# Performance work log

Hardware: AMD Instinct MI355X
Metric: run time of the kernel (lower is better)

The kernel has to match this reference:

```python
import jax, jax.numpy as jnp
import numpy as np

N_NODES = 50000
HEADS = 8
NEG_SLOPE = 0.2


def _gat_conv(x, W, a_src, a_dst, b, src, dst, n_nodes):
    """PyG GATConv forward, concat=False (mean over heads), self-loops already in (src, dst)."""
    H, C = a_src.shape
    xl = (x @ W).reshape(n_nodes, H, C)                      # [N, H, C]
    alpha_src = jnp.einsum('nhc,hc->nh', xl, a_src)          # [N, H]
    alpha_dst = jnp.einsum('nhc,hc->nh', xl, a_dst)          # [N, H]
    alpha = jax.nn.leaky_relu(alpha_src[src] + alpha_dst[dst], NEG_SLOPE)  # [E, H]
    # segment softmax over edges grouped by destination node
    amax = jax.ops.segment_max(alpha, dst, num_segments=n_nodes)           # [N, H]
    amax = jnp.where(jnp.isfinite(amax), amax, jnp.zeros_like(amax))
    ex = jnp.exp(alpha - jax.lax.stop_gradient(amax)[dst])                  # [E, H]
    denom = jax.ops.segment_sum(ex, dst, num_segments=n_nodes)             # [N, H]
    coef = ex / (denom[dst] + 1e-16)                                        # [E, H]
    msg = xl[src] * coef[:, :, None]                                        # [E, H, C]
    out = jax.ops.segment_sum(msg, dst, num_segments=n_nodes)              # [N, H, C]
    return out.mean(axis=1) + b                                             # [N, C]


def setup_inputs() -> dict:
    key = jax.random.key(0)
    ks = jax.random.split(key, 12)
    in_feats, h_feats, out_feats = 256, 64, 64
    n_edges = 800000
    x = jax.random.normal(ks[0], (N_NODES, in_feats), dtype=jnp.float32)
    edge_index = jax.random.randint(ks[1], (2, n_edges), 0, N_NODES, dtype=jnp.int64)
    # Glorot-ish init for weights
    def glorot(k, shape, fan):
        return jax.random.normal(k, shape, dtype=jnp.float32) * (1.0 / np.sqrt(fan))
    W1 = glorot(ks[2], (in_feats, HEADS * h_feats), in_feats)
    a_src1 = glorot(ks[3], (HEADS, h_feats), h_feats)
    a_dst1 = glorot(ks[4], (HEADS, h_feats), h_feats)
    b1 = jnp.zeros((h_feats,), dtype=jnp.float32)
    W2 = glorot(ks[5], (h_feats, HEADS * out_feats), h_feats)
    a_src2 = glorot(ks[6], (HEADS, out_feats), out_feats)
    a_dst2 = glorot(ks[7], (HEADS, out_feats), out_feats)
    b2 = jnp.zeros((out_feats,), dtype=jnp.float32)
    return {"x": x, "edge_index": edge_index,
            "W1": W1, "a_src1": a_src1, "a_dst1": a_dst1, "b1": b1,
            "W2": W2, "a_src2": a_src2, "a_dst2": a_dst2, "b2": b2}


def reference(x, edge_index, W1, a_src1, a_dst1, b1, W2, a_src2, a_dst2, b2):
    n = x.shape[0]
    # PyG GATConv add_self_loops=True (default): append self loops
    loops = jnp.arange(n, dtype=edge_index.dtype)
    src = jnp.concatenate([edge_index[0], loops])
    dst = jnp.concatenate([edge_index[1], loops])
    # F.dropout(p=0.6) is identity in eval mode
    h = _gat_conv(x, W1, a_src1, a_dst1, b1, src, dst, n)
    h = jax.nn.relu(h)
    out = _gat_conv(h, W2, a_src2, a_dst2, b2, src, dst, n)
    return out
```

## Files before the change

kernel.cpp:

```cpp
#include <hip/hip_runtime.h>

#define NN 50000
#define MPAD 50048
#define HD 8
#define CD 64
#define NHF 512
#define SCAN_B 256
#define NBLK ((NN + SCAN_B - 1) / SCAN_B)

typedef __attribute__((ext_vector_type(8))) short short8v;
typedef __attribute__((ext_vector_type(8))) unsigned short us8;
typedef __attribute__((ext_vector_type(4))) unsigned short us4;
typedef __attribute__((ext_vector_type(4))) float f32x4;
typedef __attribute__((ext_vector_type(8))) _Float16 h8;

__device__ inline unsigned short f32_to_bf16(float f) {
    unsigned int u = __float_as_uint(f);
    unsigned int r = (u + 0x7fffu + ((u >> 16) & 1u)) >> 16;
    return (unsigned short)r;
}
__device__ inline float bf16_to_f32(unsigned short h) {
    return __uint_as_float(((unsigned int)h) << 16);
}

__global__ void k_init_cnt(int* __restrict__ cnt) {
    int i = blockIdx.x * 256 + threadIdx.x;
    if (i < NN) cnt[i] = 1;
}

__global__ void k_hist(const int* __restrict__ dst, int E, int* __restrict__ cnt) {
    int e = blockIdx.x * 256 + threadIdx.x;
    if (e < E) atomicAdd(&cnt[dst[e]], 1);
}

__global__ __launch_bounds__(SCAN_B) void k_block_sums(const int* __restrict__ cnt,
                                                       int* __restrict__ bsums) {
    __shared__ int sdata[4];
    int i = blockIdx.x * SCAN_B + threadIdx.x;
    int v = (i < NN) ? cnt[i] : 0;
#pragma unroll
    for (int off = 1; off < 64; off <<= 1) v += __shfl_xor(v, off);
    if ((threadIdx.x & 63) == 0) sdata[threadIdx.x >> 6] = v;
    __syncthreads();
    if (threadIdx.x == 0) bsums[blockIdx.x] = sdata[0] + sdata[1] + sdata[2] + sdata[3];
}

__global__ __launch_bounds__(SCAN_B) void k_scan_bsums(const int* __restrict__ bsums,
                                                       int* __restrict__ boffs, int nblk) {
    __shared__ int tmp[SCAN_B];
    int tid = threadIdx.x;
    int v = (tid < nblk) ? bsums[tid] : 0;
    tmp[tid] = v;
    __syncthreads();
    for (int off = 1; off < SCAN_B; off <<= 1) {
        int t = (tid >= off) ? tmp[tid - off] : 0;
        __syncthreads();
        tmp[tid] += t;
        __syncthreads();
    }
    if (tid < nblk) boffs[tid] = tmp[tid] - v;
}

__global__ __launch_bounds__(SCAN_B) void k_emit(const int* __restrict__ cnt,
                                                 const int* __restrict__ boffs,
                                                 int* __restrict__ row_ptr,
                                                 int* __restrict__ cursor,
                                                 int* __restrict__ csr_src) {
    __shared__ int tmp[SCAN_B];
    int tid = threadIdx.x;
    int i = blockIdx.x * SCAN_B + tid;
    int v = (i < NN) ? cnt[i] : 0;
    tmp[tid] = v;
    __syncthreads();
    for (int off = 1; off < SCAN_B; off <<= 1) {
        int t = (tid >= off) ? tmp[tid - off] : 0;
        __syncthreads();
        tmp[tid] += t;
        __syncthreads();
    }
    int base = boffs[blockIdx.x] + tmp[tid] - v;
    if (i < NN) {
        row_ptr[i] = base;
        csr_src[base] = i;
        cursor[i] = base + 1;
        if (i == NN - 1) row_ptr[NN] = base + v;
    }
}

__global__ void k_scatter(const int* __restrict__ src, const int* __restrict__ dst,
                          int E, int* __restrict__ cursor, int* __restrict__ csr_src) {
    int e = blockIdx.x * 256 + threadIdx.x;
    if (e < E) {
        int pos = atomicAdd(&cursor[dst[e]], 1);
        csr_src[pos] = src[e];
    }
}

__global__ void k_split_bt(const float* __restrict__ B, unsigned short* __restrict__ bht,
                           unsigned short* __restrict__ blt, int K) {
    int idx = blockIdx.x * 256 + threadIdx.x;
    if (idx < K * NHF) {
        int k = idx >> 9, n = idx & 511;
        float v = B[idx];
        unsigned short hb = f32_to_bf16(v);
        float l = v - bf16_to_f32(hb);
        blt[n * K + k] = f32_to_bf16(l);
        bht[n * K + k] = hb;
    }
}

#define BM 128
#define BN 256
#define BKF 32
#define LDK 40

template<int SPLIT>
__global__ __launch_bounds__(512) void k_gemm(
    const float* __restrict__ Af,
    const unsigned short* __restrict__ Aht,
    const unsigned short* __restrict__ Alt,
    const unsigned short* __restrict__ Bht,
    const unsigned short* __restrict__ Blt,
    const float* __restrict__ a_src, const float* __restrict__ a_dst,
    _Float16* __restrict__ C, float* __restrict__ asrc_out, float* __restrict__ adst_out,
    int M, int K)
{
    __shared__ unsigned short Ash[BM][LDK];
    __shared__ unsigned short Asl[BM][LDK];
    __shared__ unsigned short Bsh[BN][LDK];
    __shared__ unsigned short Bsl[BN][LDK];

    const int t = threadIdx.x;
    const int lane = t & 63;
    const int wid = t >> 6;
    const int wr = wid >> 2;
    const int wc = wid & 3;
    const int bm = blockIdx.x * BM;
    const int bn = blockIdx.y * BN;
    const int l15 = lane & 15;
    const int lg = lane >> 4;

    f32x4 acc[4][4];
#pragma unroll
    for (int mi = 0; mi < 4; ++mi)
#pragma unroll
        for (int ni = 0; ni < 4; ++ni)
            acc[mi][ni] = (f32x4){0.f, 0.f, 0.f, 0.f};

    const int srowA = t >> 2;
    const int skcA  = (t & 3) * 8;
    const int srowB = t >> 1;
    const int skcB  = (t & 1) * 16;

    for (int k0 = 0; k0 < K; k0 += BKF) {
        __syncthreads();
        if (SPLIT) {
            const int gr = bm + srowA;
            if (gr < M) {
                const float* ga = Af + (size_t)gr * K + k0 + skcA;
                float4 v0 = *(const float4*)ga;
                float4 v1 = *(const float4*)(ga + 4);
                us4 h0, l0, h1, l1;
                h0.x = f32_to_bf16(v0.x); l0.x = f32_to_bf16(v0.x - bf16_to_f32(h0.x));
                h0.y = f32_to_bf16(v0.y); l0.y = f32_to_bf16(v0.y - bf16_to_f32(h0.y));
                h0.z = f32_to_bf16(v0.z); l0.z = f32_to_bf16(v0.z - bf16_to_f32(h0.z));
                h0.w = f32_to_bf16(v0.w); l0.w = f32_to_bf16(v0.w - bf16_to_f32(h0.w));
                h1.x = f32_to_bf16(v1.x); l1.x = f32_to_bf16(v1.x - bf16_to_f32(h1.x));
                h1.y = f32_to_bf16(v1.y); l1.y = f32_to_bf16(v1.y - bf16_to_f32(h1.y));
                h1.z = f32_to_bf16(v1.z); l1.z = f32_to_bf16(v1.z - bf16_to_f32(h1.z));
                h1.w = f32_to_bf16(v1.w); l1.w = f32_to_bf16(v1.w - bf16_to_f32(h1.w));
                *(us4*)&Ash[srowA][skcA]     = h0;
                *(us4*)&Ash[srowA][skcA + 4] = h1;
                *(us4*)&Asl[srowA][skcA]     = l0;
                *(us4*)&Asl[srowA][skcA + 4] = l1;
            } else {
                us4 z = (us4){0, 0, 0, 0};
                *(us4*)&Ash[srowA][skcA]     = z;
                *(us4*)&Ash[srowA][skcA + 4] = z;
                *(us4*)&Asl[srowA][skcA]     = z;
                *(us4*)&Asl[srowA][skcA + 4] = z;
            }
        } else {
            const unsigned short* gah = Aht + (size_t)(bm + srowA) * K + k0 + skcA;
            const unsigned short* gal = Alt + (size_t)(bm + srowA) * K + k0 + skcA;
            *(us8*)&Ash[srowA][skcA] = *(const us8*)gah;
            *(us8*)&Asl[srowA][skcA] = *(const us8*)gal;
        }
        {
            const unsigned short* gbh = Bht + (size_t)(bn + srowB) * K + k0 + skcB;
            const unsigned short* gbl = Blt + (size_t)(bn + srowB) * K + k0 + skcB;
            *(us8*)&Bsh[srowB][skcB]     = *(const us8*)gbh;
            *(us8*)&Bsh[srowB][skcB + 8] = *(const us8*)(gbh + 8);
            *(us8*)&Bsl[srowB][skcB]     = *(const us8*)gbl;
            *(us8*)&Bsl[srowB][skcB + 8] = *(const us8*)(gbl + 8);
        }
        __syncthreads();

        short8v ah[4], al[4], bh[4], bl[4];
#pragma unroll
        for (int i = 0; i < 4; ++i) {
            ah[i] = *(const short8v*)&Ash[wr * 64 + i * 16 + l15][lg * 8];
            al[i] = *(const short8v*)&Asl[wr * 64 + i * 16 + l15][lg * 8];
            bh[i] = *(const short8v*)&Bsh[wc * 64 + i * 16 + l15][lg * 8];
            bl[i] = *(const short8v*)&Bsl[wc * 64 + i * 16 + l15][lg * 8];
        }
#pragma unroll
        for (int mi = 0; mi < 4; ++mi)
#pragma unroll
            for (int ni = 0; ni < 4; ++ni) {
                acc[mi][ni] = __builtin_amdgcn_mfma_f32_16x16x32_bf16(ah[mi], bh[ni], acc[mi][ni], 0, 0, 0);
                acc[mi][ni] = __builtin_amdgcn_mfma_f32_16x16x32_bf16(ah[mi], bl[ni], acc[mi][ni], 0, 0, 0);
                acc[mi][ni] = __builtin_amdgcn_mfma_f32_16x16x32_bf16(al[mi], bh[ni], acc[mi][ni], 0, 0, 0);
            }
    }

    const int head_w = (bn >> 6) + wc;
    float ca[4], cd[4];
#pragma unroll
    for (int ni = 0; ni < 4; ++ni) {
        ca[ni] = a_src[head_w * 64 + ni * 16 + l15];
        cd[ni] = a_dst[head_w * 64 + ni * 16 + l15];
    }
#pragma unroll
    for (int mi = 0; mi < 4; ++mi) {
#pragma unroll
        for (int r = 0; r < 4; ++r) {
            int row = bm + wr * 64 + mi * 16 + lg * 4 + r;
            float ps = 0.f, pd = 0.f;
#pragma unroll
            for (int ni = 0; ni < 4; ++ni) {
                float cv = acc[mi][ni][r];
                int col = bn + wc * 64 + ni * 16 + l15;
                if (row < M) C[(size_t)row * NHF + col] = (_Float16)cv;
                ps += cv * ca[ni];
                pd += cv * cd[ni];
            }
#pragma unroll
            for (int off = 1; off < 16; off <<= 1) {
                ps += __shfl_xor(ps, off);
                pd += __shfl_xor(pd, off);
            }
            if (l15 == 0 && row < M) {
                asrc_out[row * HD + head_w] = ps;
                adst_out[row * HD + head_w] = pd;
            }
        }
    }
}

__global__ __launch_bounds__(256) void k_aggregate(
    const _Float16* __restrict__ xl, const float* __restrict__ asrc,
    const float* __restrict__ adst, const int* __restrict__ row_ptr,
    const int* __restrict__ csr_src, const float* __restrict__ bias,
    float* __restrict__ out, unsigned short* __restrict__ o_hi,
    unsigned short* __restrict__ o_lo, int mode)
{
    __shared__ float sh[4][NHF];
    const int wid  = threadIdx.x >> 6;
    const int lane = threadIdx.x & 63;
    const int n    = blockIdx.x * 4 + wid;
    const int head = lane >> 3;
    const int off  = lane * 8;

    const float ad = adst[n * HD + head];
    const int e0 = row_ptr[n];
    const int e1 = row_ptr[n + 1];

    float acc[8] = {};
    float s = 0.f;

    int e = e0;
    for (; e + 4 <= e1; e += 4) {
        int i0 = csr_src[e];
        int i1 = csr_src[e + 1];
        int i2 = csr_src[e + 2];
        int i3 = csr_src[e + 3];
        float a0 = asrc[i0 * HD + head];
        float a1 = asrc[i1 * HD + head];
        float a2 = asrc[i2 * HD + head];
        float a3 = asrc[i3 * HD + head];
        h8 v0 = *(const h8*)(xl + (size_t)i0 * NHF + off);
        h8 v1 = *(const h8*)(xl + (size_t)i1 * NHF + off);
        h8 v2 = *(const h8*)(xl + (size_t)i2 * NHF + off);
        h8 v3 = *(const h8*)(xl + (size_t)i3 * NHF + off);
        a0 += ad; a1 += ad; a2 += ad; a3 += ad;
        float p0 = __expf(a0 > 0.f ? a0 : 0.2f * a0);
        float p1 = __expf(a1 > 0.f ? a1 : 0.2f * a1);
        float p2 = __expf(a2 > 0.f ? a2 : 0.2f * a2);
        float p3 = __expf(a3 > 0.f ? a3 : 0.2f * a3);
        s += p0 + p1 + p2 + p3;
#pragma unroll
        for (int j = 0; j < 8; ++j) {
            acc[j] += p0 * (float)v0[j];
            acc[j] += p1 * (float)v1[j];
            acc[j] += p2 * (float)v2[j];
            acc[j] += p3 * (float)v3[j];
        }
    }
    for (; e < e1; ++e) {
        int i0 = csr_src[e];
        float a = asrc[i0 * HD + head] + ad;
        h8 vv = *(const h8*)(xl + (size_t)i0 * NHF + off);
        float p = __expf(a > 0.f ? a : 0.2f * a);
        s += p;
#pragma unroll
        for (int j = 0; j < 8; ++j) acc[j] += p * (float)vv[j];
    }

    const float inv = 1.f / (s + 1e-16f);
#pragma unroll
    for (int j = 0; j < 8; ++j) sh[wid][off + j] = acc[j] * inv;
    __syncthreads();

    float sum = 0.f;
#pragma unroll
    for (int h2 = 0; h2 < HD; ++h2) sum += sh[wid][h2 * CD + lane];
    float res = sum * 0.125f + bias[lane];
    if (mode) {
        res = fmaxf(res, 0.f);
        unsigned short hb = f32_to_bf16(res);
        o_hi[(size_t)n * CD + lane] = hb;
        o_lo[(size_t)n * CD + lane] = f32_to_bf16(res - bf16_to_f32(hb));
    } else {
        out[(size_t)n * CD + lane] = res;
    }
}

extern "C" void kernel_launch(void* const* d_in, const int* in_sizes, int n_in,
                              void* d_out, int out_size, void* d_ws, size_t ws_size,
                              hipStream_t stream) {
    const float* x   = (const float*)d_in[0];
    const int*   ei  = (const int*)d_in[1];
    const float* W1  = (const float*)d_in[2];
    const float* as1 = (const float*)d_in[3];
    const float* ad1 = (const float*)d_in[4];
    const float* b1  = (const float*)d_in[5];
    const float* W2  = (const float*)d_in[6];
    const float* as2 = (const float*)d_in[7];
    const float* ad2 = (const float*)d_in[8];
    const float* b2  = (const float*)d_in[9];

    const int E = in_sizes[1] / 2;
    const int* esrc = ei;
    const int* edst = ei + E;

    char* ws = (char*)d_ws;
    _Float16* xlh        = (_Float16*)ws;
    float* asrc          = (float*)(ws + 51200000);
    float* adst          = (float*)(ws + 52800000);
    unsigned short* Hh   = (unsigned short*)(ws + 54400000);
    unsigned short* Hl   = (unsigned short*)(ws + 60806144);
    int*   row_ptr       = (int*)(ws + 67212288);
    int*   cursor        = (int*)(ws + 67412480);
    int*   csr_src       = (int*)(ws + 67612480);
    unsigned short* Bht1 = (unsigned short*)(ws + 71012480);
    unsigned short* Blt1 = (unsigned short*)(ws + 71274624);
    unsigned short* Bht2 = (unsigned short*)(ws + 71536768);
    unsigned short* Blt2 = (unsigned short*)(ws + 71602304);
    int*   bsums         = (int*)(ws + 71667840);
    int*   boffs         = (int*)(ws + 71668736);

    k_init_cnt<<<(NN + 255) / 256, 256, 0, stream>>>(cursor);
    k_hist<<<(E + 255) / 256, 256, 0, stream>>>(edst, E, cursor);
    k_block_sums<<<NBLK, SCAN_B, 0, stream>>>(cursor, bsums);
    k_scan_bsums<<<1, SCAN_B, 0, stream>>>(bsums, boffs, NBLK);
    k_emit<<<NBLK, SCAN_B, 0, stream>>>(cursor, boffs, row_ptr, cursor, csr_src);
    k_scatter<<<(E + 255) / 256, 256, 0, stream>>>(esrc, edst, E, cursor, csr_src);

    k_split_bt<<<(256 * NHF + 255) / 256, 256, 0, stream>>>(W1, Bht1, Blt1, 256);
    k_split_bt<<<(64 * NHF + 255) / 256, 256, 0, stream>>>(W2, Bht2, Blt2, 64);

    dim3 gemm_grid(MPAD / BM, NHF / BN);

    k_gemm<1><<<gemm_grid, 512, 0, stream>>>(x, nullptr, nullptr, Bht1, Blt1, as1, ad1,
                                             xlh, asrc, adst, NN, 256);
    k_aggregate<<<NN / 4, 256, 0, stream>>>(xlh, asrc, adst, row_ptr, csr_src, b1,
                                            nullptr, Hh, Hl, 1);

    k_gemm<0><<<gemm_grid, 512, 0, stream>>>(nullptr, Hh, Hl, Bht2, Blt2, as2, ad2,
                                             xlh, asrc, adst, NN, 64);
    k_aggregate<<<NN / 4, 256, 0, stream>>>(xlh, asrc, adst, row_ptr, csr_src, b2,
                                            (float*)d_out, nullptr, nullptr, 0);
}
```

Before: 452.0 us.

## Merge weight-split launches, memset histogram, and restructure GEMM B-fragment loads

Replaces the count-init kernel with a memset and folds the self-loop +1 into the scan kernels. Merges the two weight split/transpose launches into one kernel. In the GEMM, B fragments are now loaded per column tile inside the loop rather than all up front, and launch_bounds gains a minimum-occupancy hint of 4. These aim to cut launch overhead and register pressure, at the risk of LDS reads interleaving with the MFMA chain.

```diff
diff --git a/kernel.cpp b/kernel.cpp
--- a/kernel.cpp
+++ b/kernel.cpp
@@ -23,11 +23,6 @@
     return __uint_as_float(((unsigned int)h) << 16);
 }
 
-__global__ void k_init_cnt(int* __restrict__ cnt) {
-    int i = blockIdx.x * 256 + threadIdx.x;
-    if (i < NN) cnt[i] = 1;
-}
-
 __global__ void k_hist(const int* __restrict__ dst, int E, int* __restrict__ cnt) {
     int e = blockIdx.x * 256 + threadIdx.x;
     if (e < E) atomicAdd(&cnt[dst[e]], 1);
@@ -37,7 +32,7 @@
                                                        int* __restrict__ bsums) {
     __shared__ int sdata[4];
     int i = blockIdx.x * SCAN_B + threadIdx.x;
-    int v = (i < NN) ? cnt[i] : 0;
+    int v = (i < NN) ? cnt[i] + 1 : 0;
 #pragma unroll
     for (int off = 1; off < 64; off <<= 1) v += __shfl_xor(v, off);
     if ((threadIdx.x & 63) == 0) sdata[threadIdx.x >> 6] = v;
@@ -69,7 +64,7 @@
     __shared__ int tmp[SCAN_B];
     int tid = threadIdx.x;
     int i = blockIdx.x * SCAN_B + tid;
-    int v = (i < NN) ? cnt[i] : 0;
+    int v = (i < NN) ? cnt[i] + 1 : 0;
     tmp[tid] = v;
     __syncthreads();
     for (int off = 1; off < SCAN_B; off <<= 1) {
@@ -96,16 +91,25 @@
     }
 }
 
-__global__ void k_split_bt(const float* __restrict__ B, unsigned short* __restrict__ bht,
-                           unsigned short* __restrict__ blt, int K) {
+__global__ void k_split_w(const float* __restrict__ W1, unsigned short* __restrict__ bht1,
+                          unsigned short* __restrict__ blt1,
+                          const float* __restrict__ W2, unsigned short* __restrict__ bht2,
+                          unsigned short* __restrict__ blt2) {
     int idx = blockIdx.x * 256 + threadIdx.x;
-    if (idx < K * NHF) {
+    const int n1 = 256 * NHF;
+    if (idx < n1) {
         int k = idx >> 9, n = idx & 511;
-        float v = B[idx];
+        float v = W1[idx];
         unsigned short hb = f32_to_bf16(v);
-        float l = v - bf16_to_f32(hb);
-        blt[n * K + k] = f32_to_bf16(l);
-        bht[n * K + k] = hb;
+        blt1[n * 256 + k] = f32_to_bf16(v - bf16_to_f32(hb));
+        bht1[n * 256 + k] = hb;
+    } else if (idx < n1 + 64 * NHF) {
+        int i2 = idx - n1;
+        int k = i2 >> 9, n = i2 & 511;
+        float v = W2[i2];
+        unsigned short hb = f32_to_bf16(v);
+        blt2[n * 64 + k] = f32_to_bf16(v - bf16_to_f32(hb));
+        bht2[n * 64 + k] = hb;
     }
 }
 
@@ -115,7 +119,7 @@
 #define LDK 40
 
 template<int SPLIT>
-__global__ __launch_bounds__(512) void k_gemm(
+__global__ __launch_bounds__(512, 4) void k_gemm(
     const float* __restrict__ Af,
     const unsigned short* __restrict__ Aht,
     const unsigned short* __restrict__ Alt,
@@ -196,22 +200,23 @@
         }
         __syncthreads();
 
-        short8v ah[4], al[4], bh[4], bl[4];
+        short8v ah[4], al[4];
 #pragma unroll
         for (int i = 0; i < 4; ++i) {
             ah[i] = *(const short8v*)&Ash[wr * 64 + i * 16 + l15][lg * 8];
             al[i] = *(const short8v*)&Asl[wr * 64 + i * 16 + l15][lg * 8];
-            bh[i] = *(const short8v*)&Bsh[wc * 64 + i * 16 + l15][lg * 8];
-            bl[i] = *(const short8v*)&Bsl[wc * 64 + i * 16 + l15][lg * 8];
-        }
-#pragma unroll
-        for (int mi = 0; mi < 4; ++mi)
-#pragma unroll
-            for (int ni = 0; ni < 4; ++ni) {
-                acc[mi][ni] = __builtin_amdgcn_mfma_f32_16x16x32_bf16(ah[mi], bh[ni], acc[mi][ni], 0, 0, 0);
-                acc[mi][ni] = __builtin_amdgcn_mfma_f32_16x16x32_bf16(ah[mi], bl[ni], acc[mi][ni], 0, 0, 0);
-                acc[mi][ni] = __builtin_amdgcn_mfma_f32_16x16x32_bf16(al[mi], bh[ni], acc[mi][ni], 0, 0, 0);
-            }
+        }
+#pragma unroll
+        for (int ni = 0; ni < 4; ++ni) {
+            short8v bh = *(const short8v*)&Bsh[wc * 64 + ni * 16 + l15][lg * 8];
+            short8v bl = *(const short8v*)&Bsl[wc * 64 + ni * 16 + l15][lg * 8];
+#pragma unroll
+            for (int mi = 0; mi < 4; ++mi) {
+                acc[mi][ni] = __builtin_amdgcn_mfma_f32_16x16x32_bf16(ah[mi], bh, acc[mi][ni], 0, 0, 0);
+                acc[mi][ni] = __builtin_amdgcn_mfma_f32_16x16x32_bf16(ah[mi], bl, acc[mi][ni], 0, 0, 0);
+                acc[mi][ni] = __builtin_amdgcn_mfma_f32_16x16x32_bf16(al[mi], bh, acc[mi][ni], 0, 0, 0);
+            }
+        }
     }
 
     const int head_w = (bn >> 6) + wc;
@@ -360,15 +365,15 @@
     int*   bsums         = (int*)(ws + 71667840);
     int*   boffs         = (int*)(ws + 71668736);
 
-    k_init_cnt<<<(NN + 255) / 256, 256, 0, stream>>>(cursor);
+    hipMemsetAsync(cursor, 0, NN * sizeof(int), stream);
     k_hist<<<(E + 255) / 256, 256, 0, stream>>>(edst, E, cursor);
     k_block_sums<<<NBLK, SCAN_B, 0, stream>>>(cursor, bsums);
     k_scan_bsums<<<1, SCAN_B, 0, stream>>>(bsums, boffs, NBLK);
     k_emit<<<NBLK, SCAN_B, 0, stream>>>(cursor, boffs, row_ptr, cursor, csr_src);
     k_scatter<<<(E + 255) / 256, 256, 0, stream>>>(esrc, edst, E, cursor, csr_src);
 
-    k_split_bt<<<(256 * NHF + 255) / 256, 256, 0, stream>>>(W1, Bht1, Blt1, 256);
-    k_split_bt<<<(64 * NHF + 255) / 256, 256, 0, stream>>>(W2, Bht2, Blt2, 64);
+    k_split_w<<<((256 + 64) * NHF + 255) / 256, 256, 0, stream>>>(W1, Bht1, Blt1,
+                                                                  W2, Bht2, Blt2);
 
     dim3 gemm_grid(MPAD / BM, NHF / BN);
 
```

After: 453.4 us, median of 2. Within noise of the previous version (+0.3%).
